# Kernel tuning notes

Measured on AMD Instinct MI355X. Metric: run time of the kernel, lower is better.

Reference implementation:

```python
import jax, jax.numpy as jnp
import numpy as np

HEADS = 8


def setup_inputs() -> dict:
    key = jax.random.key(0)
    k1, k2, k3 = jax.random.split(key, 3)
    b, n, d = 4, 2048, 256
    x = jax.random.normal(k1, (b, n, d), dtype=jnp.float32)
    # torch Linear weight is [out, in]; we store transposed [in, out] for x @ W
    w_qkv = jax.random.normal(k2, (d, 3 * d), dtype=jnp.float32) * (d ** -0.5)
    b_qkv = jnp.zeros((3 * d,), dtype=jnp.float32)
    w_out = jax.random.normal(k3, (d, d), dtype=jnp.float32) * (d ** -0.5)
    b_out = jnp.zeros((d,), dtype=jnp.float32)
    return {"x": x, "w_qkv": w_qkv, "b_qkv": b_qkv, "w_out": w_out, "b_out": b_out}


def reference(x, w_qkv, b_qkv, w_out, b_out):
    b, n, d = x.shape
    h = HEADS
    dh = d // h
    scale = d ** -0.5  # NOTE: original scales by full dim**-0.5, not head_dim
    qkv = x @ w_qkv + b_qkv                      # [b, n, 3d]
    q, k, v = jnp.split(qkv, 3, axis=-1)         # each [b, n, d]
    to_heads = lambda t: t.reshape(b, n, h, dh).transpose(0, 2, 1, 3)  # [b,h,n,dh]
    q, k, v = to_heads(q), to_heads(k), to_heads(v)
    dots = jnp.einsum('bhid,bhjd->bhij', q, k) * scale   # [b,h,n,n]
    attn = jax.nn.softmax(dots, axis=-1)
    out = jnp.einsum('bhij,bhjd->bhid', attn, v)         # [b,h,n,dh]
    out = out.transpose(0, 2, 1, 3).reshape(b, n, d)     # [b,n,d]
    return out @ w_out + b_out  # dropout is identity in eval mode
```

## Files before the change

kernel.cpp:

```cpp
#include <hip/hip_runtime.h>
#include <hip/hip_bf16.h>
#include <math.h>

#define BATCH  4
#define SEQ    2048
#define DMODEL 256
#define NH     8
#define DH     32
#define MTOT   (BATCH*SEQ)
#define QSCALE 0.09016844005556021f

typedef short  bf16x8 __attribute__((ext_vector_type(8)));
typedef float  f32x4  __attribute__((ext_vector_type(4)));

static __device__ __forceinline__ ushort f2bf(float f) {
    __hip_bfloat16 h = __float2bfloat16(f);
    return __builtin_bit_cast(ushort, h);
}

static __device__ __forceinline__ uint rne2(float a, float b) {
    uint ua = __builtin_bit_cast(uint, a);
    uint ub = __builtin_bit_cast(uint, b);
    ua += 0x7FFFu + ((ua >> 16) & 1u);
    ub += 0x7FFFu + ((ub >> 16) & 1u);
    return __builtin_amdgcn_perm(ub, ua, 0x07060302);
}

__global__ __launch_bounds__(256) void wcvt_all(
    const float* __restrict__ wq, const float* __restrict__ wo,
    ushort* __restrict__ wqT, ushort* __restrict__ woT)
{
    __shared__ float T[32][33];
    const int t = threadIdx.x;
    const int bx = blockIdx.x;
    const float* w; ushort* wT; int N, n0;
    if (bx < 24) { w = wq; wT = wqT; N = 768; n0 = bx * 32; }
    else         { w = wo; wT = woT; N = 256; n0 = (bx - 24) * 32; }
    const int k0 = blockIdx.y * 32;
    {
        int tr = t >> 3, tc = (t & 7) * 4;
        *(float4*)&T[tr][tc] = *(const float4*)(w + (size_t)(k0 + tr) * N + n0 + tc);
    }
    __syncthreads();
    int nl = t >> 3, kq = (t & 7) * 4;
    ushort4 pk;
    pk.x = f2bf(T[kq + 0][nl]); pk.y = f2bf(T[kq + 1][nl]);
    pk.z = f2bf(T[kq + 2][nl]); pk.w = f2bf(T[kq + 3][nl]);
    *(ushort4*)&wT[(size_t)(n0 + nl) * 256 + k0 + kq] = pk;
}

#define LSQ 72

__global__ __launch_bounds__(256, 3) void qkv_gemm(
    const float* __restrict__ x, const ushort* __restrict__ wT,
    const float* __restrict__ bias,
    ushort* __restrict__ qo, ushort* __restrict__ ko, ushort* __restrict__ vo)
{
    __shared__ ushort As[64 * LSQ];
    __shared__ ushort Bs[128 * LSQ];
    const int tid  = threadIdx.x;
    const int wid  = tid >> 6;
    const int lane = tid & 63;
    const int lq   = lane & 15;
    const int quad = lane >> 4;
    const int wm   = wid & 1;
    const int wn   = wid >> 1;
    const int m0   = blockIdx.y * 64;
    const int n0   = blockIdx.x * 128;
    const bool isV = (blockIdx.x >= 4);

    const int ar0 = tid >> 4,          ac0 = (tid & 15) * 4;
    const int ar1 = (tid + 256) >> 4,  ac1 = ac0;
    const int ar2 = (tid + 512) >> 4,  ac2 = ac0;
    const int ar3 = (tid + 768) >> 4,  ac3 = ac0;
    const int br0 = tid >> 3,          bc0 = (tid & 7) * 8;
    const int br1 = (tid + 256) >> 3,  bc1 = bc0;
    const int br2 = (tid + 512) >> 3,  bc2 = bc0;
    const int br3 = (tid + 768) >> 3,  bc3 = bc0;

    const float*  xb = x  + (size_t)m0 * 256;
    const ushort* wb = wT + (size_t)n0 * 256;

    f32x4 acc[8];
#pragma unroll
    for (int i = 0; i < 8; ++i) acc[i] = {0.f, 0.f, 0.f, 0.f};

    float4 ra0 = *(const float4*)(xb + (size_t)ar0 * 256 + ac0);
    float4 ra1 = *(const float4*)(xb + (size_t)ar1 * 256 + ac1);
    float4 ra2 = *(const float4*)(xb + (size_t)ar2 * 256 + ac2);
    float4 ra3 = *(const float4*)(xb + (size_t)ar3 * 256 + ac3);
    uint4  rb0 = *(const uint4*)(wb + (size_t)br0 * 256 + bc0);
    uint4  rb1 = *(const uint4*)(wb + (size_t)br1 * 256 + bc1);
    uint4  rb2 = *(const uint4*)(wb + (size_t)br2 * 256 + bc2);
    uint4  rb3 = *(const uint4*)(wb + (size_t)br3 * 256 + bc3);

    for (int k0 = 0; k0 < 256; k0 += 64) {
        __syncthreads();
        {
            uint2 w;
            w.x = rne2(ra0.x, ra0.y); w.y = rne2(ra0.z, ra0.w);
            *(uint2*)&As[ar0 * LSQ + ac0] = w;
            w.x = rne2(ra1.x, ra1.y); w.y = rne2(ra1.z, ra1.w);
            *(uint2*)&As[ar1 * LSQ + ac1] = w;
            w.x = rne2(ra2.x, ra2.y); w.y = rne2(ra2.z, ra2.w);
            *(uint2*)&As[ar2 * LSQ + ac2] = w;
            w.x = rne2(ra3.x, ra3.y); w.y = rne2(ra3.z, ra3.w);
            *(uint2*)&As[ar3 * LSQ + ac3] = w;
        }
        *(uint4*)&Bs[br0 * LSQ + bc0] = rb0;
        *(uint4*)&Bs[br1 * LSQ + bc1] = rb1;
        *(uint4*)&Bs[br2 * LSQ + bc2] = rb2;
        *(uint4*)&Bs[br3 * LSQ + bc3] = rb3;
        __syncthreads();

        const int kn = (k0 + 64) & 255;
        ra0 = *(const float4*)(xb + (size_t)ar0 * 256 + kn + ac0);
        ra1 = *(const float4*)(xb + (size_t)ar1 * 256 + kn + ac1);
        ra2 = *(const float4*)(xb + (size_t)ar2 * 256 + kn + ac2);
        ra3 = *(const float4*)(xb + (size_t)ar3 * 256 + kn + ac3);
        rb0 = *(const uint4*)(wb + (size_t)br0 * 256 + kn + bc0);
        rb1 = *(const uint4*)(wb + (size_t)br1 * 256 + kn + bc1);
        rb2 = *(const uint4*)(wb + (size_t)br2 * 256 + kn + bc2);
        rb3 = *(const uint4*)(wb + (size_t)br3 * 256 + kn + bc3);

#pragma unroll
        for (int kh = 0; kh < 2; ++kh) {
            bf16x8 af[2], bfg[4];
#pragma unroll
            for (int mi = 0; mi < 2; ++mi)
                af[mi]  = *(const bf16x8*)&As[(wm * 32 + mi * 16 + lq) * LSQ + kh * 32 + quad * 8];
#pragma unroll
            for (int ni = 0; ni < 4; ++ni)
                bfg[ni] = *(const bf16x8*)&Bs[(wn * 64 + ni * 16 + lq) * LSQ + kh * 32 + quad * 8];
            if (isV) {
#pragma unroll
                for (int mi = 0; mi < 2; ++mi)
#pragma unroll
                    for (int ni = 0; ni < 4; ++ni)
                        acc[mi * 4 + ni] = __builtin_amdgcn_mfma_f32_16x16x32_bf16(
                            af[mi], bfg[ni], acc[mi * 4 + ni], 0, 0, 0);
            } else {
#pragma unroll
                for (int ni = 0; ni < 4; ++ni)
#pragma unroll
                    for (int mi = 0; mi < 2; ++mi)
                        acc[ni * 2 + mi] = __builtin_amdgcn_mfma_f32_16x16x32_bf16(
                            bfg[ni], af[mi], acc[ni * 2 + mi], 0, 0, 0);
            }
        }
    }

    if (!isV) {
#pragma unroll
        for (int ni = 0; ni < 4; ++ni) {
            int nb = n0 + wn * 64 + ni * 16 + quad * 4;
            float4 bs = *(const float4*)(bias + nb);
            int h   = (nb >> 5) & 7;
            int dh0 = nb & 31;
            bool  isQ = (nb < 256);
            float sc  = isQ ? QSCALE : 1.0f;
            ushort* dst = isQ ? qo : ko;
#pragma unroll
            for (int mi = 0; mi < 2; ++mi) {
                int m   = m0 + wm * 32 + mi * 16 + lq;
                int b   = m >> 11, seq = m & 2047;
                f32x4 c = acc[ni * 2 + mi];
                ushort4 pk;
                pk.x = f2bf((c[0] + bs.x) * sc); pk.y = f2bf((c[1] + bs.y) * sc);
                pk.z = f2bf((c[2] + bs.z) * sc); pk.w = f2bf((c[3] + bs.w) * sc);
                *(ushort4*)&dst[(((size_t)b * NH + h) * SEQ + seq) * DH + dh0] = pk;
            }
        }
    } else {
#pragma unroll
        for (int ni = 0; ni < 4; ++ni) {
            int n  = n0 + wn * 64 + ni * 16 + lq;
            int h  = (n >> 5) & 7;
            int dh = n & 31;
            float bsc = bias[n];
#pragma unroll
            for (int mi = 0; mi < 2; ++mi) {
                int mb  = m0 + wm * 32 + mi * 16 + quad * 4;
                int b   = mb >> 11, seq = mb & 2047;
                f32x4 c = acc[mi * 4 + ni];
                ushort4 pk;
                pk.x = f2bf(c[0] + bsc); pk.y = f2bf(c[1] + bsc);
                pk.z = f2bf(c[2] + bsc); pk.w = f2bf(c[3] + bsc);
                *(ushort4*)&vo[(((size_t)b * NH + h) * DH + dh) * SEQ + seq] = pk;
            }
        }
    }
}

#define KS_STRIDE 40
#define VT_STRIDE 136
#define P_STRIDE  136

__global__ __launch_bounds__(256, 4) void attn_mfma(
    const ushort* __restrict__ qb, const ushort* __restrict__ kb,
    const ushort* __restrict__ vtb, ushort* __restrict__ a_bf)
{
    __shared__ ushort Ks[128 * KS_STRIDE];
    __shared__ ushort VsT[32 * VT_STRIDE];
    __shared__ ushort Pl[4 * 16 * P_STRIDE];

    const int tid  = threadIdx.x;
    const int wid  = tid >> 6;
    const int lane = tid & 63;
    const int lq   = lane & 15;
    const int quad = lane >> 4;
    const int h    = blockIdx.y;
    const int b    = blockIdx.z;
    const int bh   = b * NH + h;
    const int q0   = blockIdx.x * 64 + wid * 16;

    const ushort* qrow = qb + ((size_t)bh * SEQ + q0 + lq) * DH + quad * 8;
    const bf16x8 qf = *(const bf16x8*)qrow;

    const ushort* kbase  = kb  + (size_t)bh * SEQ * DH;
    const ushort* vtbase = vtb + (size_t)bh * DH * SEQ;
    ushort* Pw = Pl + wid * 16 * P_STRIDE;

    const int f0 = tid, f1 = tid + 256;
    const int kgo0 = (f0 >> 2) * DH + (f0 & 3) * 8;
    const int kgo1 = (f1 >> 2) * DH + (f1 & 3) * 8;
    const int klo0 = (f0 >> 2) * KS_STRIDE + (f0 & 3) * 8;
    const int klo1 = (f1 >> 2) * KS_STRIDE + (f1 & 3) * 8;
    const int vgo0 = (f0 >> 4) * SEQ + (f0 & 15) * 8;
    const int vgo1 = (f1 >> 4) * SEQ + (f1 & 15) * 8;
    const int vlo0 = (f0 >> 4) * VT_STRIDE + (f0 & 15) * 8;
    const int vlo1 = (f1 >> 4) * VT_STRIDE + (f1 & 15) * 8;

    uint4 kr0 = *(const uint4*)(kbase  + kgo0);
    uint4 kr1 = *(const uint4*)(kbase  + kgo1);
    uint4 vr0 = *(const uint4*)(vtbase + vgo0);
    uint4 vr1 = *(const uint4*)(vtbase + vgo1);

    f32x4 o0 = {0.f, 0.f, 0.f, 0.f};
    f32x4 o1 = {0.f, 0.f, 0.f, 0.f};
    float l = 0.f;

    for (int kt = 0; kt < SEQ; kt += 128) {
        __syncthreads();
        *(uint4*)&Ks[klo0]  = kr0;
        *(uint4*)&Ks[klo1]  = kr1;
        *(uint4*)&VsT[vlo0] = vr0;
        *(uint4*)&VsT[vlo1] = vr1;
        __syncthreads();

        {
            const int ktn = (kt + 128) & (SEQ - 1);
            const ushort* kn = kbase  + (size_t)ktn * DH;
            const ushort* vn = vtbase + ktn;
            kr0 = *(const uint4*)(kn + kgo0);
            kr1 = *(const uint4*)(kn + kgo1);
            vr0 = *(const uint4*)(vn + vgo0);
            vr1 = *(const uint4*)(vn + vgo1);
        }

        f32x4 st[8];
#pragma unroll
        for (int t = 0; t < 8; ++t) {
            bf16x8 kf = *(const bf16x8*)&Ks[(t * 16 + lq) * KS_STRIDE + quad * 8];
            f32x4 z = {0.f, 0.f, 0.f, 0.f};
            st[t] = __builtin_amdgcn_mfma_f32_16x16x32_bf16(kf, qf, z, 0, 0, 0);
        }

#pragma unroll
        for (int t = 0; t < 8; ++t) {
            float p0 = __builtin_amdgcn_exp2f(st[t][0]);
            float p1 = __builtin_amdgcn_exp2f(st[t][1]);
            float p2 = __builtin_amdgcn_exp2f(st[t][2]);
            float p3 = __builtin_amdgcn_exp2f(st[t][3]);
            l += (p0 + p1) + (p2 + p3);
            uint2 w;
            w.x = rne2(p0, p1);
            w.y = rne2(p2, p3);
            *(uint2*)&Pw[lq * P_STRIDE + t * 16 + quad * 4] = w;
        }

#pragma unroll
        for (int s = 0; s < 4; ++s) {
            bf16x8 pf = *(const bf16x8*)&Pw[lq * P_STRIDE + s * 32 + quad * 8];
            bf16x8 v0 = *(const bf16x8*)&VsT[lq        * VT_STRIDE + s * 32 + quad * 8];
            bf16x8 v1 = *(const bf16x8*)&VsT[(16 + lq) * VT_STRIDE + s * 32 + quad * 8];
            o0 = __builtin_amdgcn_mfma_f32_16x16x32_bf16(v0, pf, o0, 0, 0, 0);
            o1 = __builtin_amdgcn_mfma_f32_16x16x32_bf16(v1, pf, o1, 0, 0, 0);
        }
    }

    l += __shfl_xor(l, 16);
    l += __shfl_xor(l, 32);
    float inv = 1.0f / l;
    ushort* dst = a_bf + ((size_t)b * SEQ + q0 + lq) * DMODEL + h * DH;
    uint2 w0, w1;
    w0.x = rne2(o0[0] * inv, o0[1] * inv);
    w0.y = rne2(o0[2] * inv, o0[3] * inv);
    w1.x = rne2(o1[0] * inv, o1[1] * inv);
    w1.y = rne2(o1[2] * inv, o1[3] * inv);
    *(uint2*)&dst[quad * 4]      = w0;
    *(uint2*)&dst[16 + quad * 4] = w1;
}

__global__ __launch_bounds__(256) void out_gemm(
    const ushort* __restrict__ a, const ushort* __restrict__ wT,
    const float* __restrict__ bias, float* __restrict__ out)
{
    __shared__ ushort As[64 * LSQ];
    __shared__ ushort Bs[64 * LSQ];
    const int tid  = threadIdx.x;
    const int wid  = tid >> 6;
    const int lane = tid & 63;
    const int lq   = lane & 15;
    const int quad = lane >> 4;
    const int wm   = wid & 1;
    const int wn   = wid >> 1;
    const int m0   = blockIdx.y * 64;
    const int n0   = blockIdx.x * 64;

    const int f0 = tid, f1 = tid + 256;
    const int r0 = f0 >> 3, c0 = (f0 & 7) * 8;
    const int r1 = f1 >> 3, c1 = (f1 & 7) * 8;

    const ushort* ab = a  + (size_t)m0 * 256;
    const ushort* wb = wT + (size_t)n0 * 256;

    f32x4 acc[4];
#pragma unroll
    for (int i = 0; i < 4; ++i) acc[i] = {0.f, 0.f, 0.f, 0.f};

    uint4 ra0 = *(const uint4*)(ab + (size_t)r0 * 256 + c0);
    uint4 ra1 = *(const uint4*)(ab + (size_t)r1 * 256 + c1);
    uint4 rb0 = *(const uint4*)(wb + (size_t)r0 * 256 + c0);
    uint4 rb1 = *(const uint4*)(wb + (size_t)r1 * 256 + c1);

    for (int k0 = 0; k0 < 256; k0 += 64) {
        __syncthreads();
        *(uint4*)&As[r0 * LSQ + c0] = ra0;
        *(uint4*)&As[r1 * LSQ + c1] = ra1;
        *(uint4*)&Bs[r0 * LSQ + c0] = rb0;
        *(uint4*)&Bs[r1 * LSQ + c1] = rb1;
        __syncthreads();

        const int kn = (k0 + 64) & 255;
        ra0 = *(const uint4*)(ab + (size_t)r0 * 256 + kn + c0);
        ra1 = *(const uint4*)(ab + (size_t)r1 * 256 + kn + c1);
        rb0 = *(const uint4*)(wb + (size_t)r0 * 256 + kn + c0);
        rb1 = *(const uint4*)(wb + (size_t)r1 * 256 + kn + c1);

#pragma unroll
        for (int kh = 0; kh < 2; ++kh) {
            bf16x8 af[2], bfg[2];
#pragma unroll
            for (int mi = 0; mi < 2; ++mi)
                af[mi]  = *(const bf16x8*)&As[(wm * 32 + mi * 16 + lq) * LSQ + kh * 32 + quad * 8];
#pragma unroll
            for (int ni = 0; ni < 2; ++ni)
                bfg[ni] = *(const bf16x8*)&Bs[(wn * 32 + ni * 16 + lq) * LSQ + kh * 32 + quad * 8];
#pragma unroll
            for (int ni = 0; ni < 2; ++ni)
#pragma unroll
                for (int mi = 0; mi < 2; ++mi)
                    acc[ni * 2 + mi] = __builtin_amdgcn_mfma_f32_16x16x32_bf16(
                        bfg[ni], af[mi], acc[ni * 2 + mi], 0, 0, 0);
        }
    }

#pragma unroll
    for (int ni = 0; ni < 2; ++ni) {
        int nb = n0 + wn * 32 + ni * 16 + quad * 4;
        float4 bs = *(const float4*)(bias + nb);
#pragma unroll
        for (int mi = 0; mi < 2; ++mi) {
            int m = m0 + wm * 32 + mi * 16 + lq;
            f32x4 c = acc[ni * 2 + mi];
            float4 o;
            o.x = c[0] + bs.x; o.y = c[1] + bs.y;
            o.z = c[2] + bs.z; o.w = c[3] + bs.w;
            *(float4*)&out[(size_t)m * DMODEL + nb] = o;
        }
    }
}

extern "C" void kernel_launch(void* const* d_in, const int* in_sizes, int n_in,
                              void* d_out, int out_size, void* d_ws, size_t ws_size,
                              hipStream_t stream) {
    const float* x     = (const float*)d_in[0];
    const float* w_qkv = (const float*)d_in[1];
    const float* b_qkv = (const float*)d_in[2];
    const float* w_out = (const float*)d_in[3];
    const float* b_out = (const float*)d_in[4];
    float* out = (float*)d_out;

    const size_t TSZ = (size_t)MTOT * DMODEL;
    ushort* q_ws = (ushort*)d_ws;
    ushort* k_ws = q_ws + TSZ;
    ushort* v_ws = k_ws + TSZ;
    ushort* a_bf = v_ws + TSZ;
    ushort* wqT  = a_bf + TSZ;
    ushort* woT  = wqT + 768 * 256;

    wcvt_all<<<dim3(32, 8), 256, 0, stream>>>(w_qkv, w_out, wqT, woT);
    qkv_gemm<<<dim3(6, 128), 256, 0, stream>>>(x, wqT, b_qkv, q_ws, k_ws, v_ws);
    attn_mfma<<<dim3(SEQ / 64, NH, BATCH), 256, 0, stream>>>(
        q_ws, k_ws, v_ws, a_bf);
    out_gemm<<<dim3(4, 128), 256, 0, stream>>>(a_bf, woT, b_out, out);
}
```

Baseline: 131.1 us.

## Double query rows per attention warp and pre-convert x to bf16

Each attention warp now handles 32 query rows instead of 16, so every K and V tile staged in shared memory is reused across twice as many queries. The grid is halved and the P buffer doubled. Separately, x is converted to bf16 once in the weight-conversion kernel, so the QKV GEMM no longer rounds activations six times (once per column block) and reads half the bytes. This adds an extra intermediate buffer and write pass, and it raises register and LDS pressure in the attention kernel, which could reduce occupancy.

```diff
diff --git a/kernel.cpp b/kernel.cpp
--- a/kernel.cpp
+++ b/kernel.cpp
@@ -28,11 +28,28 @@
 
 __global__ __launch_bounds__(256) void wcvt_all(
     const float* __restrict__ wq, const float* __restrict__ wo,
-    ushort* __restrict__ wqT, ushort* __restrict__ woT)
+    const float* __restrict__ x,
+    ushort* __restrict__ wqT, ushort* __restrict__ woT,
+    ushort* __restrict__ xbf)
 {
+    const int t  = threadIdx.x;
+    const int bx = blockIdx.x;
+    if (bx >= 32) {
+        const size_t base = ((size_t)(bx - 32) * 8 + blockIdx.y) * 4096 + t * 16;
+        float4 f0 = *(const float4*)(x + base);
+        float4 f1 = *(const float4*)(x + base + 4);
+        float4 f2 = *(const float4*)(x + base + 8);
+        float4 f3 = *(const float4*)(x + base + 12);
+        uint4 w0, w1;
+        w0.x = rne2(f0.x, f0.y); w0.y = rne2(f0.z, f0.w);
+        w0.z = rne2(f1.x, f1.y); w0.w = rne2(f1.z, f1.w);
+        w1.x = rne2(f2.x, f2.y); w1.y = rne2(f2.z, f2.w);
+        w1.z = rne2(f3.x, f3.y); w1.w = rne2(f3.z, f3.w);
+        *(uint4*)&xbf[base]     = w0;
+        *(uint4*)&xbf[base + 8] = w1;
+        return;
+    }
     __shared__ float T[32][33];
-    const int t = threadIdx.x;
-    const int bx = blockIdx.x;
     const float* w; ushort* wT; int N, n0;
     if (bx < 24) { w = wq; wT = wqT; N = 768; n0 = bx * 32; }
     else         { w = wo; wT = woT; N = 256; n0 = (bx - 24) * 32; }
@@ -52,7 +69,7 @@
 #define LSQ 72
 
 __global__ __launch_bounds__(256, 3) void qkv_gemm(
-    const float* __restrict__ x, const ushort* __restrict__ wT,
+    const ushort* __restrict__ xb_, const ushort* __restrict__ wT,
     const float* __restrict__ bias,
     ushort* __restrict__ qo, ushort* __restrict__ ko, ushort* __restrict__ vo)
 {
@@ -69,44 +86,31 @@
     const int n0   = blockIdx.x * 128;
     const bool isV = (blockIdx.x >= 4);
 
-    const int ar0 = tid >> 4,          ac0 = (tid & 15) * 4;
-    const int ar1 = (tid + 256) >> 4,  ac1 = ac0;
-    const int ar2 = (tid + 512) >> 4,  ac2 = ac0;
-    const int ar3 = (tid + 768) >> 4,  ac3 = ac0;
-    const int br0 = tid >> 3,          bc0 = (tid & 7) * 8;
-    const int br1 = (tid + 256) >> 3,  bc1 = bc0;
-    const int br2 = (tid + 512) >> 3,  bc2 = bc0;
-    const int br3 = (tid + 768) >> 3,  bc3 = bc0;
-
-    const float*  xb = x  + (size_t)m0 * 256;
-    const ushort* wb = wT + (size_t)n0 * 256;
+    const int ar0 = tid >> 3,         ac0 = (tid & 7) * 8;
+    const int ar1 = (tid + 256) >> 3, ac1 = ac0;
+    const int br0 = tid >> 3,         bc0 = (tid & 7) * 8;
+    const int br1 = (tid + 256) >> 3, bc1 = bc0;
+    const int br2 = (tid + 512) >> 3, bc2 = bc0;
+    const int br3 = (tid + 768) >> 3, bc3 = bc0;
+
+    const ushort* xb = xb_ + (size_t)m0 * 256;
+    const ushort* wb = wT  + (size_t)n0 * 256;
 
     f32x4 acc[8];
 #pragma unroll
     for (int i = 0; i < 8; ++i) acc[i] = {0.f, 0.f, 0.f, 0.f};
 
-    float4 ra0 = *(const float4*)(xb + (size_t)ar0 * 256 + ac0);
-    float4 ra1 = *(const float4*)(xb + (size_t)ar1 * 256 + ac1);
-    float4 ra2 = *(const float4*)(xb + (size_t)ar2 * 256 + ac2);
-    float4 ra3 = *(const float4*)(xb + (size_t)ar3 * 256 + ac3);
-    uint4  rb0 = *(const uint4*)(wb + (size_t)br0 * 256 + bc0);
-    uint4  rb1 = *(const uint4*)(wb + (size_t)br1 * 256 + bc1);
-    uint4  rb2 = *(const uint4*)(wb + (size_t)br2 * 256 + bc2);
-    uint4  rb3 = *(const uint4*)(wb + (size_t)br3 * 256 + bc3);
+    uint4 ra0 = *(const uint4*)(xb + (size_t)ar0 * 256 + ac0);
+    uint4 ra1 = *(const uint4*)(xb + (size_t)ar1 * 256 + ac1);
+    uint4 rb0 = *(const uint4*)(wb + (size_t)br0 * 256 + bc0);
+    uint4 rb1 = *(const uint4*)(wb + (size_t)br1 * 256 + bc1);
+    uint4 rb2 = *(const uint4*)(wb + (size_t)br2 * 256 + bc2);
+    uint4 rb3 = *(const uint4*)(wb + (size_t)br3 * 256 + bc3);
 
     for (int k0 = 0; k0 < 256; k0 += 64) {
         __syncthreads();
-        {
-            uint2 w;
-            w.x = rne2(ra0.x, ra0.y); w.y = rne2(ra0.z, ra0.w);
-            *(uint2*)&As[ar0 * LSQ + ac0] = w;
-            w.x = rne2(ra1.x, ra1.y); w.y = rne2(ra1.z, ra1.w);
-            *(uint2*)&As[ar1 * LSQ + ac1] = w;
-            w.x = rne2(ra2.x, ra2.y); w.y = rne2(ra2.z, ra2.w);
-            *(uint2*)&As[ar2 * LSQ + ac2] = w;
-            w.x = rne2(ra3.x, ra3.y); w.y = rne2(ra3.z, ra3.w);
-            *(uint2*)&As[ar3 * LSQ + ac3] = w;
-        }
+        *(uint4*)&As[ar0 * LSQ + ac0] = ra0;
+        *(uint4*)&As[ar1 * LSQ + ac1] = ra1;
         *(uint4*)&Bs[br0 * LSQ + bc0] = rb0;
         *(uint4*)&Bs[br1 * LSQ + bc1] = rb1;
         *(uint4*)&Bs[br2 * LSQ + bc2] = rb2;
@@ -114,10 +118,8 @@
         __syncthreads();
 
         const int kn = (k0 + 64) & 255;
-        ra0 = *(const float4*)(xb + (size_t)ar0 * 256 + kn + ac0);
-        ra1 = *(const float4*)(xb + (size_t)ar1 * 256 + kn + ac1);
-        ra2 = *(const float4*)(xb + (size_t)ar2 * 256 + kn + ac2);
-        ra3 = *(const float4*)(xb + (size_t)ar3 * 256 + kn + ac3);
+        ra0 = *(const uint4*)(xb + (size_t)ar0 * 256 + kn + ac0);
+        ra1 = *(const uint4*)(xb + (size_t)ar1 * 256 + kn + ac1);
         rb0 = *(const uint4*)(wb + (size_t)br0 * 256 + kn + bc0);
         rb1 = *(const uint4*)(wb + (size_t)br1 * 256 + kn + bc1);
         rb2 = *(const uint4*)(wb + (size_t)br2 * 256 + kn + bc2);
@@ -202,7 +204,7 @@
 {
     __shared__ ushort Ks[128 * KS_STRIDE];
     __shared__ ushort VsT[32 * VT_STRIDE];
-    __shared__ ushort Pl[4 * 16 * P_STRIDE];
+    __shared__ ushort Pl[4 * 32 * P_STRIDE];
 
     const int tid  = threadIdx.x;
     const int wid  = tid >> 6;
@@ -212,14 +214,15 @@
     const int h    = blockIdx.y;
     const int b    = blockIdx.z;
     const int bh   = b * NH + h;
-    const int q0   = blockIdx.x * 64 + wid * 16;
-
-    const ushort* qrow = qb + ((size_t)bh * SEQ + q0 + lq) * DH + quad * 8;
-    const bf16x8 qf = *(const bf16x8*)qrow;
+    const int q0   = blockIdx.x * 128 + wid * 32;
+
+    const ushort* qbase = qb + ((size_t)bh * SEQ + q0) * DH;
+    const bf16x8 qf0 = *(const bf16x8*)(qbase + (size_t)lq * DH + quad * 8);
+    const bf16x8 qf1 = *(const bf16x8*)(qbase + (size_t)(16 + lq) * DH + quad * 8);
 
     const ushort* kbase  = kb  + (size_t)bh * SEQ * DH;
     const ushort* vtbase = vtb + (size_t)bh * DH * SEQ;
-    ushort* Pw = Pl + wid * 16 * P_STRIDE;
+    ushort* Pw = Pl + wid * 32 * P_STRIDE;
 
     const int f0 = tid, f1 = tid + 256;
     const int kgo0 = (f0 >> 2) * DH + (f0 & 3) * 8;
@@ -238,7 +241,9 @@
 
     f32x4 o0 = {0.f, 0.f, 0.f, 0.f};
     f32x4 o1 = {0.f, 0.f, 0.f, 0.f};
-    float l = 0.f;
+    f32x4 o2 = {0.f, 0.f, 0.f, 0.f};
+    f32x4 o3 = {0.f, 0.f, 0.f, 0.f};
+    float l0 = 0.f, l1 = 0.f;
 
     for (int kt = 0; kt < SEQ; kt += 128) {
         __syncthreads();
@@ -258,48 +263,81 @@
             vr1 = *(const uint4*)(vn + vgo1);
         }
 
-        f32x4 st[8];
-#pragma unroll
-        for (int t = 0; t < 8; ++t) {
-            bf16x8 kf = *(const bf16x8*)&Ks[(t * 16 + lq) * KS_STRIDE + quad * 8];
-            f32x4 z = {0.f, 0.f, 0.f, 0.f};
-            st[t] = __builtin_amdgcn_mfma_f32_16x16x32_bf16(kf, qf, z, 0, 0, 0);
-        }
-
-#pragma unroll
-        for (int t = 0; t < 8; ++t) {
-            float p0 = __builtin_amdgcn_exp2f(st[t][0]);
-            float p1 = __builtin_amdgcn_exp2f(st[t][1]);
-            float p2 = __builtin_amdgcn_exp2f(st[t][2]);
-            float p3 = __builtin_amdgcn_exp2f(st[t][3]);
-            l += (p0 + p1) + (p2 + p3);
-            uint2 w;
-            w.x = rne2(p0, p1);
-            w.y = rne2(p2, p3);
-            *(uint2*)&Pw[lq * P_STRIDE + t * 16 + quad * 4] = w;
+        {
+            f32x4 st[8];
+#pragma unroll
+            for (int t = 0; t < 8; ++t) {
+                bf16x8 kf = *(const bf16x8*)&Ks[(t * 16 + lq) * KS_STRIDE + quad * 8];
+                f32x4 z = {0.f, 0.f, 0.f, 0.f};
+                st[t] = __builtin_amdgcn_mfma_f32_16x16x32_bf16(kf, qf0, z, 0, 0, 0);
+            }
+#pragma unroll
+            for (int t = 0; t < 8; ++t) {
+                float p0 = __builtin_amdgcn_exp2f(st[t][0]);
+                float p1 = __builtin_amdgcn_exp2f(st[t][1]);
+                float p2 = __builtin_amdgcn_exp2f(st[t][2]);
+                float p3 = __builtin_amdgcn_exp2f(st[t][3]);
+                l0 += (p0 + p1) + (p2 + p3);
+                uint2 w;
+                w.x = rne2(p0, p1);
+                w.y = rne2(p2, p3);
+                *(uint2*)&Pw[lq * P_STRIDE + t * 16 + quad * 4] = w;
+            }
+        }
+        {
+            f32x4 st[8];
+#pragma unroll
+            for (int t = 0; t < 8; ++t) {
+                bf16x8 kf = *(const bf16x8*)&Ks[(t * 16 + lq) * KS_STRIDE + quad * 8];
+                f32x4 z = {0.f, 0.f, 0.f, 0.f};
+                st[t] = __builtin_amdgcn_mfma_f32_16x16x32_bf16(kf, qf1, z, 0, 0, 0);
+            }
+#pragma unroll
+            for (int t = 0; t < 8; ++t) {
+                float p0 = __builtin_amdgcn_exp2f(st[t][0]);
+                float p1 = __builtin_amdgcn_exp2f(st[t][1]);
+                float p2 = __builtin_amdgcn_exp2f(st[t][2]);
+                float p3 = __builtin_amdgcn_exp2f(st[t][3]);
+                l1 += (p0 + p1) + (p2 + p3);
+                uint2 w;
+                w.x = rne2(p0, p1);
+                w.y = rne2(p2, p3);
+                *(uint2*)&Pw[(16 + lq) * P_STRIDE + t * 16 + quad * 4] = w;
+            }
         }
 
 #pragma unroll
         for (int s = 0; s < 4; ++s) {
-            bf16x8 pf = *(const bf16x8*)&Pw[lq * P_STRIDE + s * 32 + quad * 8];
             bf16x8 v0 = *(const bf16x8*)&VsT[lq        * VT_STRIDE + s * 32 + quad * 8];
             bf16x8 v1 = *(const bf16x8*)&VsT[(16 + lq) * VT_STRIDE + s * 32 + quad * 8];
-            o0 = __builtin_amdgcn_mfma_f32_16x16x32_bf16(v0, pf, o0, 0, 0, 0);
-            o1 = __builtin_amdgcn_mfma_f32_16x16x32_bf16(v1, pf, o1, 0, 0, 0);
-        }
-    }
-
-    l += __shfl_xor(l, 16);
-    l += __shfl_xor(l, 32);
-    float inv = 1.0f / l;
-    ushort* dst = a_bf + ((size_t)b * SEQ + q0 + lq) * DMODEL + h * DH;
+            bf16x8 p0 = *(const bf16x8*)&Pw[lq        * P_STRIDE + s * 32 + quad * 8];
+            bf16x8 p1 = *(const bf16x8*)&Pw[(16 + lq) * P_STRIDE + s * 32 + quad * 8];
+            o0 = __builtin_amdgcn_mfma_f32_16x16x32_bf16(v0, p0, o0, 0, 0, 0);
+            o1 = __builtin_amdgcn_mfma_f32_16x16x32_bf16(v1, p0, o1, 0, 0, 0);
+            o2 = __builtin_amdgcn_mfma_f32_16x16x32_bf16(v0, p1, o2, 0, 0, 0);
+            o3 = __builtin_amdgcn_mfma_f32_16x16x32_bf16(v1, p1, o3, 0, 0, 0);
+        }
+    }
+
+    l0 += __shfl_xor(l0, 16); l0 += __shfl_xor(l0, 32);
+    l1 += __shfl_xor(l1, 16); l1 += __shfl_xor(l1, 32);
+    float inv0 = 1.0f / l0;
+    float inv1 = 1.0f / l1;
+    ushort* dst0 = a_bf + ((size_t)b * SEQ + q0 + lq) * DMODEL + h * DH;
+    ushort* dst1 = dst0 + 16 * DMODEL;
     uint2 w0, w1;
-    w0.x = rne2(o0[0] * inv, o0[1] * inv);
-    w0.y = rne2(o0[2] * inv, o0[3] * inv);
-    w1.x = rne2(o1[0] * inv, o1[1] * inv);
-    w1.y = rne2(o1[2] * inv, o1[3] * inv);
-    *(uint2*)&dst[quad * 4]      = w0;
-    *(uint2*)&dst[16 + quad * 4] = w1;
+    w0.x = rne2(o0[0] * inv0, o0[1] * inv0);
+    w0.y = rne2(o0[2] * inv0, o0[3] * inv0);
+    w1.x = rne2(o1[0] * inv0, o1[1] * inv0);
+    w1.y = rne2(o1[2] * inv0, o1[3] * inv0);
+    *(uint2*)&dst0[quad * 4]      = w0;
+    *(uint2*)&dst0[16 + quad * 4] = w1;
+    w0.x = rne2(o2[0] * inv1, o2[1] * inv1);
+    w0.y = rne2(o2[2] * inv1, o2[3] * inv1);
+    w1.x = rne2(o3[0] * inv1, o3[1] * inv1);
+    w1.y = rne2(o3[2] * inv1, o3[3] * inv1);
+    *(uint2*)&dst1[quad * 4]      = w0;
+    *(uint2*)&dst1[16 + quad * 4] = w1;
 }
 
 __global__ __launch_bounds__(256) void out_gemm(
@@ -397,12 +435,13 @@
     ushort* k_ws = q_ws + TSZ;
     ushort* v_ws = k_ws + TSZ;
     ushort* a_bf = v_ws + TSZ;
-    ushort* wqT  = a_bf + TSZ;
+    ushort* xbf  = a_bf + TSZ;
+    ushort* wqT  = xbf + TSZ;
     ushort* woT  = wqT + 768 * 256;
 
-    wcvt_all<<<dim3(32, 8), 256, 0, stream>>>(w_qkv, w_out, wqT, woT);
-    qkv_gemm<<<dim3(6, 128), 256, 0, stream>>>(x, wqT, b_qkv, q_ws, k_ws, v_ws);
-    attn_mfma<<<dim3(SEQ / 64, NH, BATCH), 256, 0, stream>>>(
+    wcvt_all<<<dim3(96, 8), 256, 0, stream>>>(w_qkv, w_out, x, wqT, woT, xbf);
+    qkv_gemm<<<dim3(6, 128), 256, 0, stream>>>(xbf, wqT, b_qkv, q_ws, k_ws, v_ws);
+    attn_mfma<<<dim3(SEQ / 128, NH, BATCH), 256, 0, stream>>>(
         q_ws, k_ws, v_ws, a_bf);
     out_gemm<<<dim3(4, 128), 256, 0, stream>>>(a_bf, woT, b_out, out);
 }
```

After: 124.2 us. 1.06x faster.
